# Kernel optimization log

Measured on AMD Instinct MI355X. Metric: run time of the kernel, lower is better.

## Reference

```python
import jax, jax.numpy as jnp
import numpy as np


def _keras_lstm_cell(x, h_tm1, c_tm1, k, rk, b):
    # Keras LSTMCell math: gates ordered i, f, c(g), o
    z = x @ k + h_tm1 @ rk + b  # [B, 4H]
    i, f, g, o = jnp.split(z, 4, axis=-1)
    i = jax.nn.sigmoid(i)
    f = jax.nn.sigmoid(f)
    c = f * c_tm1 + i * jnp.tanh(g)
    h = jax.nn.sigmoid(o) * jnp.tanh(c)
    return h, c


def setup_inputs() -> dict:
    key = jax.random.key(0)
    k1, k2, k3, k4 = jax.random.split(key, 4)
    T, B, H, L = 30, 256, 1024, 4
    inputs = jax.random.normal(k1, (T, B, H), dtype=jnp.float32)
    # scale weights to avoid gate saturation across 30 steps
    kernel = jax.random.normal(k2, (L, H, 4 * H), dtype=jnp.float32) * 0.05
    rec_kernel = jax.random.normal(k3, (L, H, 4 * H), dtype=jnp.float32) * 0.05
    bias = jax.random.normal(k4, (L, 4 * H), dtype=jnp.float32) * 0.05
    return {"inputs": inputs, "kernel": kernel, "rec_kernel": rec_kernel, "bias": bias}


def reference(inputs, kernel, rec_kernel, bias):
    # Faithful to the TF source: it passes (c, h) where Keras expects (h, c),
    # a self-consistent swap across steps, EXCEPT `cur_input = h` actually
    # feeds the Keras cell state c to the next layer. We reproduce that.
    T, B, H = inputs.shape
    L = kernel.shape[0]
    h0 = jnp.zeros((L, B, H), dtype=inputs.dtype)  # keras hidden per layer
    c0 = jnp.zeros((L, B, H), dtype=inputs.dtype)  # keras cell per layer

    def step(carry, x_t):
        hs, cs = carry
        cur = x_t
        new_h, new_c = [], []
        for j in range(L):
            h_new, c_new = _keras_lstm_cell(cur, hs[j], cs[j], kernel[j], rec_kernel[j], bias[j])
            cur = c_new  # source feeds its "h" (== keras cell state) onward
            new_h.append(h_new)
            new_c.append(c_new)
        return (jnp.stack(new_h), jnp.stack(new_c)), cur

    (_, _), outs = jax.lax.scan(step, (h0, c0), inputs)
    return outs[-1]  # final cur_input after the last timestep, shape [B, H]
```

## Files before the change

### kernel.cpp

```cpp
#include <hip/hip_runtime.h>
#include <hip/hip_fp16.h>

typedef _Float16 half8 __attribute__((ext_vector_type(8)));
typedef float floatx4 __attribute__((ext_vector_type(4)));

#define T_STEPS 30
#define BATCH   256
#define HID     1024
#define LAYERS  4
#define N4H     4096
#define K2      2048

#define BM 128
#define BN 128
#define BKH 64
#define KITERS 16
#define ZLD 132

#define AS1(p) ((const __attribute__((address_space(1))) void*)(p))
#define AS3(p) ((__attribute__((address_space(3))) void*)(p))

__global__ void transpose_weights(const float* __restrict__ Wk,
                                  const float* __restrict__ Wr,
                                  _Float16* __restrict__ wrt) {
    __shared__ float tile[64][33];
    const int zc = blockIdx.z;
    const int j = zc >> 1, mat = zc & 1;
    const float* src = (mat == 0 ? Wk : Wr) + (size_t)j * HID * N4H;
    _Float16* dst = wrt + (size_t)j * N4H * K2 + mat * HID;
    const int c0 = blockIdx.x * 32;
    const int k0 = blockIdx.y * 64;
    const int tx = threadIdx.x, ty = threadIdx.y;
    #pragma unroll
    for (int i = 0; i < 8; ++i)
        tile[ty + i * 8][tx] = src[(size_t)(k0 + ty + i * 8) * N4H + (c0 + tx)];
    __syncthreads();
    const int tid = ty * 32 + tx;
    const int kk = tid & 63, cb = tid >> 6;
    #pragma unroll
    for (int jj = 0; jj < 8; ++jj) {
        const int cp = cb * 8 + jj;
        const int c = c0 + cp;
        const int q = ((c & (HID - 1)) << 2) | (c >> 10);
        dst[(size_t)q * K2 + (k0 + kk)] = (_Float16)tile[kk][cp];
    }
}

__global__ void cvt_inputs(const float* __restrict__ in, _Float16* __restrict__ out) {
    const size_t i = ((size_t)blockIdx.x * 256 + threadIdx.x) * 8;
    const float4 a = *(const float4*)(in + i);
    const float4 b = *(const float4*)(in + i + 4);
    half8 v;
    v[0] = (_Float16)a.x; v[1] = (_Float16)a.y; v[2] = (_Float16)a.z; v[3] = (_Float16)a.w;
    v[4] = (_Float16)b.x; v[5] = (_Float16)b.y; v[6] = (_Float16)b.z; v[7] = (_Float16)b.w;
    *(half8*)(out + i) = v;
}

__global__ __launch_bounds__(512) void lstm_diag(
    const _Float16* __restrict__ Xf,
    _Float16*       __restrict__ c_act,
    _Float16*       __restrict__ h_act,
    const _Float16* __restrict__ WRt,
    const float*    __restrict__ bias,
    float*          __restrict__ c_master,
    int diag, int packed_t, int packed_j)
{
    const int z = blockIdx.z;
    const int t = (packed_t >> (8 * z)) & 255;
    const int j = (packed_j >> (8 * z)) & 255;
    const size_t BH = (size_t)BATCH * HID;

    const _Float16* X    = (j == 0) ? (Xf + (size_t)t * BH)
                                    : (c_act + ((size_t)((diag - 1) & 1) * LAYERS + (j - 1)) * BH);
    const _Float16* Hrec = h_act + (size_t)j * BH;
    const _Float16* WR   = WRt + (size_t)j * N4H * K2;
    const float* bias_j  = bias + (size_t)j * N4H;
    float* c_m           = c_master + (size_t)j * BH;
    _Float16* c_out      = c_act + ((size_t)(diag & 1) * LAYERS + j) * BH;
    _Float16* h_out      = h_act + (size_t)j * BH;

    __shared__ __align__(16) char smem[131072];
    float* zs = (float*)smem;

    const int tid  = threadIdx.x;
    const int w    = tid >> 6, lane = tid & 63;
    const int quad = lane >> 4, l16 = lane & 15;
    const int h    = w >> 2;
    const int sp   = w & 3;
    const int mw   = (sp & 1) * 64;
    const int nw   = (sp >> 1) * 64;
    const int m0   = blockIdx.y * BM;
    const int q0   = blockIdx.x * BN;
    const int th   = tid & 255;
    const int wbase = (w & 3) * 64;

    const _Float16* Ag0 = h ? Hrec : X;
    const _Float16* Bg0 = WR + h * HID;

    floatx4 acc[4][4];
    #pragma unroll
    for (int a = 0; a < 4; ++a)
        #pragma unroll
        for (int b = 0; b < 4; ++b)
            #pragma unroll
            for (int e = 0; e < 4; ++e) acc[a][b][e] = 0.f;

#define STAGE(bufsel, kc_) do {                                                         \
        _Float16* As_ = (_Float16*)(smem + (bufsel) * 65536 + h * 32768);               \
        _Float16* Bs_ = As_ + 8192;                                                     \
        const _Float16* Agk = Ag0 + (kc_);                                              \
        const _Float16* Bgk = Bg0 + (kc_);                                              \
        _Pragma("unroll")                                                               \
        for (int i_ = 0; i_ < 4; ++i_) {                                                \
            const int slot = i_ * 256 + th;                                             \
            const int r_ = slot >> 3;                                                   \
            const int g_ = (slot & 7) ^ (r_ & 7);                                       \
            __builtin_amdgcn_global_load_lds(AS1(Agk + (size_t)(m0 + r_) * HID + g_ * 8),\
                                             AS3(As_ + (i_ * 256 + wbase) * 8), 16, 0, 0);\
        }                                                                               \
        _Pragma("unroll")                                                               \
        for (int i_ = 0; i_ < 4; ++i_) {                                                \
            const int slot = i_ * 256 + th;                                             \
            const int q_ = slot >> 3;                                                   \
            const int g_ = (slot & 7) ^ (q_ & 7);                                       \
            __builtin_amdgcn_global_load_lds(AS1(Bgk + (size_t)(q0 + q_) * K2 + g_ * 8), \
                                             AS3(Bs_ + (i_ * 256 + wbase) * 8), 16, 0, 0);\
        }                                                                               \
    } while (0)

#define COMPUTE(bufsel) do {                                                            \
        const _Float16* As_ = (const _Float16*)(smem + (bufsel) * 65536 + h * 32768);   \
        const _Float16* Bs_ = As_ + 8192;                                               \
        _Pragma("unroll")                                                               \
        for (int ks = 0; ks < 2; ++ks) {                                                \
            const int gq = ks * 4 + quad;                                               \
            half8 bfrag[4];                                                             \
            _Pragma("unroll")                                                           \
            for (int b = 0; b < 4; ++b) {                                               \
                const int q = nw + b * 16 + l16;                                        \
                bfrag[b] = *(const half8*)&Bs_[((q << 3) + (gq ^ (q & 7))) * 8];        \
            }                                                                           \
            _Pragma("unroll")                                                           \
            for (int a = 0; a < 4; ++a) {                                               \
                const int r = mw + a * 16 + l16;                                        \
                const half8 afrag = *(const half8*)&As_[((r << 3) + (gq ^ (r & 7))) * 8];\
                acc[a][0] = __builtin_amdgcn_mfma_f32_16x16x32_f16(afrag, bfrag[0], acc[a][0], 0, 0, 0);\
                acc[a][1] = __builtin_amdgcn_mfma_f32_16x16x32_f16(afrag, bfrag[1], acc[a][1], 0, 0, 0);\
                acc[a][2] = __builtin_amdgcn_mfma_f32_16x16x32_f16(afrag, bfrag[2], acc[a][2], 0, 0, 0);\
                acc[a][3] = __builtin_amdgcn_mfma_f32_16x16x32_f16(afrag, bfrag[3], acc[a][3], 0, 0, 0);\
            }                                                                           \
        }                                                                               \
    } while (0)

    STAGE(0, 0);
    __syncthreads();
    #pragma unroll 2
    for (int ts = 0; ts < KITERS; ++ts) {
        const int cur = ts & 1;
        if (ts + 1 < KITERS) STAGE(cur ^ 1, (ts + 1) * BKH);
        COMPUTE(cur);
        __syncthreads();
    }

    if (h == 0) {
        #pragma unroll
        for (int a = 0; a < 4; ++a)
            #pragma unroll
            for (int b = 0; b < 4; ++b)
                #pragma unroll
                for (int e = 0; e < 4; ++e)
                    zs[(mw + a * 16 + quad * 4 + e) * ZLD + nw + b * 16 + l16] = acc[a][b][e];
    }
    __syncthreads();
    if (h == 1) {
        #pragma unroll
        for (int a = 0; a < 4; ++a)
            #pragma unroll
            for (int b = 0; b < 4; ++b)
                #pragma unroll
                for (int e = 0; e < 4; ++e)
                    zs[(mw + a * 16 + quad * 4 + e) * ZLD + nw + b * 16 + l16] += acc[a][b][e];
    }
    __syncthreads();

    const int nl = tid & 31;
    const int mb = tid >> 5;
    const int n  = blockIdx.x * 32 + nl;
    const float bi = bias_j[n];
    const float bf = bias_j[HID + n];
    const float bg = bias_j[2 * HID + n];
    const float bo = bias_j[3 * HID + n];
    #pragma unroll
    for (int mi = 0; mi < 8; ++mi) {
        const int ml = mb + mi * 16;
        const int m  = m0 + ml;
        const float4 z4 = *(const float4*)&zs[ml * ZLD + 4 * nl];
        const float zi = z4.x + bi;
        const float zf = z4.y + bf;
        const float zg = z4.z + bg;
        const float zo = z4.w + bo;
        const float ig = 1.f / (1.f + __expf(-zi));
        const float fg = 1.f / (1.f + __expf(-zf));
        const float gg = tanhf(zg);
        const float og = 1.f / (1.f + __expf(-zo));
        const size_t idx = (size_t)m * HID + n;
        const float c = fg * c_m[idx] + ig * gg;
        const float hh = og * tanhf(c);
        c_m[idx] = c;
        c_out[idx] = (_Float16)c;
        h_out[idx] = (_Float16)hh;
    }
#undef STAGE
#undef COMPUTE
}

extern "C" void kernel_launch(void* const* d_in, const int* in_sizes, int n_in,
                              void* d_out, int out_size, void* d_ws, size_t ws_size,
                              hipStream_t stream) {
    const float* inputs     = (const float*)d_in[0];
    const float* kernel_    = (const float*)d_in[1];
    const float* rec_kernel = (const float*)d_in[2];
    const float* bias       = (const float*)d_in[3];
    float* out = (float*)d_out;

    char* ws = (char*)d_ws;
    _Float16* WRt      = (_Float16*)(ws);
    _Float16* Xf       = (_Float16*)(ws + 67108864);
    float*    c_master = (float*)   (ws + 82837504);
    _Float16* c_f16    = (_Float16*)(ws + 87031808);
    _Float16* h_f16    = (_Float16*)(ws + 91226112);

    const size_t BH = (size_t)BATCH * HID;

    hipMemsetAsync(c_master, 0, LAYERS * BH * sizeof(float), stream);
    hipMemsetAsync(h_f16, 0, LAYERS * BH * sizeof(_Float16), stream);

    transpose_weights<<<dim3(N4H / 32, HID / 64, LAYERS * 2), dim3(32, 8), 0, stream>>>(
        kernel_, rec_kernel, WRt);
    cvt_inputs<<<(T_STEPS * BATCH * HID) / 8 / 256, 256, 0, stream>>>(inputs, Xf);

    for (int d = 0; d < T_STEPS + LAYERS - 1; ++d) {
        const int jlo = (d - (T_STEPS - 1)) > 0 ? (d - (T_STEPS - 1)) : 0;
        const int jhi = d < (LAYERS - 1) ? d : (LAYERS - 1);
        const int nc  = jhi - jlo + 1;
        int pt = 0, pj = 0;
        for (int zz = 0; zz < nc; ++zz) {
            const int j = jlo + zz, tt = d - j;
            pt |= tt << (8 * zz);
            pj |= j << (8 * zz);
        }
        lstm_diag<<<dim3(N4H / BN, BATCH / BM, nc), 512, 0, stream>>>(
            Xf, c_f16, h_f16, WRt, bias, c_master, d, pt, pj);
    }

    hipMemcpyAsync(out, c_master + 3 * BH, BH * sizeof(float),
                   hipMemcpyDeviceToDevice, stream);
}
```

Measured before the change: 1.095 ms.

## Deepen GEMM K-pipeline to four LDS stages and vectorize weight transpose

```diff
diff --git a/kernel.cpp b/kernel.cpp
--- a/kernel.cpp
+++ b/kernel.cpp
@@ -13,8 +13,8 @@
 
 #define BM 128
 #define BN 128
-#define BKH 64
-#define KITERS 16
+#define BKH 32
+#define KITERS 32
 #define ZLD 132
 
 #define AS1(p) ((const __attribute__((address_space(1))) void*)(p))
@@ -23,26 +23,35 @@
 __global__ void transpose_weights(const float* __restrict__ Wk,
                                   const float* __restrict__ Wr,
                                   _Float16* __restrict__ wrt) {
-    __shared__ float tile[64][33];
+    __shared__ float tile[64][65];
     const int zc = blockIdx.z;
     const int j = zc >> 1, mat = zc & 1;
     const float* src = (mat == 0 ? Wk : Wr) + (size_t)j * HID * N4H;
     _Float16* dst = wrt + (size_t)j * N4H * K2 + mat * HID;
-    const int c0 = blockIdx.x * 32;
+    const int c0 = blockIdx.x * 64;
     const int k0 = blockIdx.y * 64;
-    const int tx = threadIdx.x, ty = threadIdx.y;
-    #pragma unroll
-    for (int i = 0; i < 8; ++i)
-        tile[ty + i * 8][tx] = src[(size_t)(k0 + ty + i * 8) * N4H + (c0 + tx)];
-    __syncthreads();
-    const int tid = ty * 32 + tx;
-    const int kk = tid & 63, cb = tid >> 6;
-    #pragma unroll
-    for (int jj = 0; jj < 8; ++jj) {
-        const int cp = cb * 8 + jj;
+    const int t = threadIdx.x;
+    const int c4 = (t & 15) * 4, lr = t >> 4;
+    #pragma unroll
+    for (int i = 0; i < 4; ++i) {
+        const float4 v = *(const float4*)(src + (size_t)(k0 + lr + i * 16) * N4H + c0 + c4);
+        tile[lr + i * 16][c4 + 0] = v.x;
+        tile[lr + i * 16][c4 + 1] = v.y;
+        tile[lr + i * 16][c4 + 2] = v.z;
+        tile[lr + i * 16][c4 + 3] = v.w;
+    }
+    __syncthreads();
+    const int kg = t & 7, cl0 = t >> 3;
+    #pragma unroll
+    for (int i = 0; i < 2; ++i) {
+        const int cp = cl0 + i * 32;
         const int c = c0 + cp;
         const int q = ((c & (HID - 1)) << 2) | (c >> 10);
-        dst[(size_t)q * K2 + (k0 + kk)] = (_Float16)tile[kk][cp];
+        half8 v;
+        #pragma unroll
+        for (int jj = 0; jj < 8; ++jj)
+            v[jj] = (_Float16)tile[kg * 8 + jj][cp];
+        *(half8*)(dst + (size_t)q * K2 + k0 + kg * 8) = v;
     }
 }
 
@@ -106,61 +115,86 @@
             for (int e = 0; e < 4; ++e) acc[a][b][e] = 0.f;
 
 #define STAGE(bufsel, kc_) do {                                                         \
-        _Float16* As_ = (_Float16*)(smem + (bufsel) * 65536 + h * 32768);               \
-        _Float16* Bs_ = As_ + 8192;                                                     \
+        _Float16* As_ = (_Float16*)(smem + (bufsel) * 32768 + h * 16384);               \
+        _Float16* Bs_ = As_ + 4096;                                                     \
         const _Float16* Agk = Ag0 + (kc_);                                              \
         const _Float16* Bgk = Bg0 + (kc_);                                              \
         _Pragma("unroll")                                                               \
-        for (int i_ = 0; i_ < 4; ++i_) {                                                \
+        for (int i_ = 0; i_ < 2; ++i_) {                                                \
             const int slot = i_ * 256 + th;                                             \
-            const int r_ = slot >> 3;                                                   \
-            const int g_ = (slot & 7) ^ (r_ & 7);                                       \
+            const int r_ = slot >> 2;                                                   \
+            const int g_ = (slot & 3) ^ (r_ & 3);                                       \
             __builtin_amdgcn_global_load_lds(AS1(Agk + (size_t)(m0 + r_) * HID + g_ * 8),\
                                              AS3(As_ + (i_ * 256 + wbase) * 8), 16, 0, 0);\
         }                                                                               \
         _Pragma("unroll")                                                               \
-        for (int i_ = 0; i_ < 4; ++i_) {                                                \
+        for (int i_ = 0; i_ < 2; ++i_) {                                                \
             const int slot = i_ * 256 + th;                                             \
-            const int q_ = slot >> 3;                                                   \
-            const int g_ = (slot & 7) ^ (q_ & 7);                                       \
+            const int q_ = slot >> 2;                                                   \
+            const int g_ = (slot & 3) ^ (q_ & 3);                                       \
             __builtin_amdgcn_global_load_lds(AS1(Bgk + (size_t)(q0 + q_) * K2 + g_ * 8), \
                                              AS3(Bs_ + (i_ * 256 + wbase) * 8), 16, 0, 0);\
         }                                                                               \
     } while (0)
 
 #define COMPUTE(bufsel) do {                                                            \
-        const _Float16* As_ = (const _Float16*)(smem + (bufsel) * 65536 + h * 32768);   \
-        const _Float16* Bs_ = As_ + 8192;                                               \
-        _Pragma("unroll")                                                               \
-        for (int ks = 0; ks < 2; ++ks) {                                                \
-            const int gq = ks * 4 + quad;                                               \
-            half8 bfrag[4];                                                             \
-            _Pragma("unroll")                                                           \
-            for (int b = 0; b < 4; ++b) {                                               \
-                const int q = nw + b * 16 + l16;                                        \
-                bfrag[b] = *(const half8*)&Bs_[((q << 3) + (gq ^ (q & 7))) * 8];        \
-            }                                                                           \
-            _Pragma("unroll")                                                           \
-            for (int a = 0; a < 4; ++a) {                                               \
-                const int r = mw + a * 16 + l16;                                        \
-                const half8 afrag = *(const half8*)&As_[((r << 3) + (gq ^ (r & 7))) * 8];\
-                acc[a][0] = __builtin_amdgcn_mfma_f32_16x16x32_f16(afrag, bfrag[0], acc[a][0], 0, 0, 0);\
-                acc[a][1] = __builtin_amdgcn_mfma_f32_16x16x32_f16(afrag, bfrag[1], acc[a][1], 0, 0, 0);\
-                acc[a][2] = __builtin_amdgcn_mfma_f32_16x16x32_f16(afrag, bfrag[2], acc[a][2], 0, 0, 0);\
-                acc[a][3] = __builtin_amdgcn_mfma_f32_16x16x32_f16(afrag, bfrag[3], acc[a][3], 0, 0, 0);\
-            }                                                                           \
-        }                                                                               \
+        const _Float16* As_ = (const _Float16*)(smem + (bufsel) * 32768 + h * 16384);   \
+        const _Float16* Bs_ = As_ + 4096;                                               \
+        half8 bfrag[4];                                                                 \
+        _Pragma("unroll")                                                               \
+        for (int b = 0; b < 4; ++b) {                                                   \
+            const int q = nw + b * 16 + l16;                                            \
+            bfrag[b] = *(const half8*)&Bs_[((q << 2) + (quad ^ (q & 3))) * 8];          \
+        }                                                                               \
+        _Pragma("unroll")                                                               \
+        for (int a = 0; a < 4; ++a) {                                                   \
+            const int r = mw + a * 16 + l16;                                            \
+            const half8 afrag = *(const half8*)&As_[((r << 2) + (quad ^ (r & 3))) * 8]; \
+            acc[a][0] = __builtin_amdgcn_mfma_f32_16x16x32_f16(afrag, bfrag[0], acc[a][0], 0, 0, 0);\
+            acc[a][1] = __builtin_amdgcn_mfma_f32_16x16x32_f16(afrag, bfrag[1], acc[a][1], 0, 0, 0);\
+            acc[a][2] = __builtin_amdgcn_mfma_f32_16x16x32_f16(afrag, bfrag[2], acc[a][2], 0, 0, 0);\
+            acc[a][3] = __builtin_amdgcn_mfma_f32_16x16x32_f16(afrag, bfrag[3], acc[a][3], 0, 0, 0);\
+        }                                                                               \
+    } while (0)
+
+#define W8 asm volatile("s_waitcnt vmcnt(8)" ::: "memory")
+#define W4 asm volatile("s_waitcnt vmcnt(4)" ::: "memory")
+#define W0 asm volatile("s_waitcnt vmcnt(0)" ::: "memory")
+
+#define STEPS(cb_, sb_, sk_, WAITER) do {                                               \
+        WAITER;                                                                         \
+        __builtin_amdgcn_s_barrier();                                                   \
+        __builtin_amdgcn_sched_barrier(0);                                              \
+        STAGE(sb_, sk_);                                                                \
+        __builtin_amdgcn_s_setprio(1);                                                  \
+        COMPUTE(cb_);                                                                   \
+        __builtin_amdgcn_s_setprio(0);                                                  \
+    } while (0)
+#define STEPN(cb_, WAITER) do {                                                         \
+        WAITER;                                                                         \
+        __builtin_amdgcn_s_barrier();                                                   \
+        __builtin_amdgcn_sched_barrier(0);                                              \
+        __builtin_amdgcn_s_setprio(1);                                                  \
+        COMPUTE(cb_);                                                                   \
+        __builtin_amdgcn_s_setprio(0);                                                  \
     } while (0)
 
     STAGE(0, 0);
-    __syncthreads();
-    #pragma unroll 2
-    for (int ts = 0; ts < KITERS; ++ts) {
-        const int cur = ts & 1;
-        if (ts + 1 < KITERS) STAGE(cur ^ 1, (ts + 1) * BKH);
-        COMPUTE(cur);
-        __syncthreads();
-    }
+    STAGE(1, BKH);
+    STAGE(2, 2 * BKH);
+
+    for (int tb = 0; tb < KITERS - 4; tb += 4) {
+        const int kc = (tb + 3) * BKH;
+        STEPS(0, 3, kc,           W8);
+        STEPS(1, 0, kc + BKH,     W8);
+        STEPS(2, 1, kc + 2 * BKH, W8);
+        STEPS(3, 2, kc + 3 * BKH, W8);
+    }
+    STEPS(0, 3, (KITERS - 1) * BKH, W8);
+    STEPN(1, W8);
+    STEPN(2, W4);
+    STEPN(3, W0);
+    __syncthreads();
 
     if (h == 0) {
         #pragma unroll
@@ -212,6 +246,11 @@
     }
 #undef STAGE
 #undef COMPUTE
+#undef STEPS
+#undef STEPN
+#undef W8
+#undef W4
+#undef W0
 }
 
 extern "C" void kernel_launch(void* const* d_in, const int* in_sizes, int n_in,
@@ -235,7 +274,7 @@
     hipMemsetAsync(c_master, 0, LAYERS * BH * sizeof(float), stream);
     hipMemsetAsync(h_f16, 0, LAYERS * BH * sizeof(_Float16), stream);
 
-    transpose_weights<<<dim3(N4H / 32, HID / 64, LAYERS * 2), dim3(32, 8), 0, stream>>>(
+    transpose_weights<<<dim3(N4H / 64, HID / 64, LAYERS * 2), 256, 0, stream>>>(
         kernel_, rec_kernel, WRt);
     cvt_inputs<<<(T_STEPS * BATCH * HID) / 8 / 256, 256, 0, stream>>>(inputs, Xf);
 
@@ -245,9 +284,9 @@
         const int nc  = jhi - jlo + 1;
         int pt = 0, pj = 0;
         for (int zz = 0; zz < nc; ++zz) {
-            const int j = jlo + zz, tt = d - j;
+            const int jj = jlo + zz, tt = d - jj;
             pt |= tt << (8 * zz);
-            pj |= j << (8 * zz);
+            pj |= jj << (8 * zz);
         }
         lstm_diag<<<dim3(N4H / BN, BATCH / BM, nc), 512, 0, stream>>>(
             Xf, c_f16, h_f16, WRt, bias, c_master, d, pt, pj);
```

Result: slower. 1.189 ms (+8.6%).
